# Optimization experiments

Measured on AMD Instinct MI355X. Metric: run time of the kernel, lower is better.

Reference implementation:

```python
import jax, jax.numpy as jnp
import numpy as np

N_NODES = 50000
N_EDGES = 800000
IN_CH = 128
HID_CH = 128
OUT_CH = 64
K = 25
LRELU_SLOPE = 0.01  # torch.nn.LeakyReLU default
NORM_EPS = 1e-12    # F.normalize default eps


def setup_inputs() -> dict:
    key = jax.random.key(0)
    ks = jax.random.split(key, 8)
    x = jax.random.normal(ks[0], (N_NODES, IN_CH), dtype=jnp.float32)
    edge_index = jax.random.randint(ks[1], (2, N_EDGES), 0, N_NODES, dtype=jnp.int32)
    # ChebConv per-order weights [K, in, hid] + bias
    W = jax.random.normal(ks[2], (K, IN_CH, HID_CH), dtype=jnp.float32) / np.sqrt(IN_CH)
    b = jax.random.normal(ks[3], (HID_CH,), dtype=jnp.float32) * 0.01
    # mu / logstd linear heads
    w_mu = jax.random.normal(ks[4], (HID_CH, OUT_CH), dtype=jnp.float32) / np.sqrt(HID_CH)
    b_mu = jax.random.normal(ks[5], (OUT_CH,), dtype=jnp.float32) * 0.01
    w_ls = jax.random.normal(ks[6], (HID_CH, OUT_CH), dtype=jnp.float32) / np.sqrt(HID_CH)
    b_ls = jax.random.normal(ks[7], (OUT_CH,), dtype=jnp.float32) * 0.01
    return {"x": x, "edge_index": edge_index, "W": W, "b": b,
            "w_mu": w_mu, "b_mu": b_mu, "w_ls": w_ls, "b_ls": b_ls}


def _cheb_conv(x, edge_index, W, b):
    # PyG ChebConv with normalization='sym', lambda_max=2.0:
    # scaled Laplacian L~ = L - I = -D^{-1/2} A D^{-1/2} (diagonal nets to zero)
    src, dst = edge_index[0], edge_index[1]
    deg = jax.ops.segment_sum(jnp.ones(src.shape[0], x.dtype), src, num_segments=x.shape[0])
    dis = jnp.where(deg > 0, jax.lax.rsqrt(jnp.where(deg > 0, deg, 1.0)), 0.0)
    enorm = -dis[src] * dis[dst]  # [E]

    def prop(h):  # out[i] = sum_{(j->i)} enorm_e * h[j]
        return jax.ops.segment_sum(enorm[:, None] * h[src], dst, num_segments=h.shape[0])

    tx0 = x
    tx1 = prop(x)
    out0 = tx0 @ W[0] + tx1 @ W[1]

    def step(carry, Wk):
        t1, t0, acc = carry
        t2 = 2.0 * prop(t1) - t0  # Chebyshev recurrence
        return (t2, t1, acc + t2 @ Wk), None

    (_, _, out), _ = jax.lax.scan(step, (tx1, tx0, out0), W[2:])
    return out + b


def reference(x, edge_index, W, b, w_mu, b_mu, w_ls, b_ls):
    h = _cheb_conv(x, edge_index, W, b)
    # eval mode: dropout is identity
    h = jnp.where(h > 0, h, LRELU_SLOPE * h)
    mu = h @ w_mu + b_mu
    ls = h @ w_ls + b_ls
    nrm = jnp.sqrt(jnp.sum(ls * ls, axis=1, keepdims=True))
    logstd = ls / jnp.maximum(nrm, NORM_EPS) * 1.8
    zeta = mu  # eval-mode reparam returns mu
    return (mu, logstd, zeta)
```

## Files before the change

### kernel.cpp

```cpp
#include <hip/hip_runtime.h>
#include <hip/hip_fp16.h>

#define N_NODES 50000
#define N_EDGES 800000
#define CH 128
#define OUT_CH 64
#define K_ORD 25
#define SLICE ((size_t)N_NODES * CH)

typedef __attribute__((ext_vector_type(8))) short s16x8;
typedef __attribute__((ext_vector_type(4))) float f32x4;

union U4H8 { uint4 u; __half2 h2[4]; ushort us[8]; };

__global__ void count_kernel(const int* __restrict__ ei, float* __restrict__ deg,
                             int* __restrict__ indeg, int E) {
    int e = blockIdx.x * blockDim.x + threadIdx.x;
    if (e >= E) return;
    int s = ei[e];
    int d = ei[E + e];
    atomicAdd(&deg[s], 1.0f);
    atomicAdd(&indeg[d], 1);
}

__global__ __launch_bounds__(256) void scan1_kernel(const int* __restrict__ indeg,
                                                    int* __restrict__ loc,
                                                    int* __restrict__ bsum, int n) {
    __shared__ int tmp[256];
    int tid = threadIdx.x;
    int i = blockIdx.x * 256 + tid;
    int v = (i < n) ? indeg[i] : 0;
    tmp[tid] = v;
    __syncthreads();
    for (int off = 1; off < 256; off <<= 1) {
        int t = (tid >= off) ? tmp[tid - off] : 0;
        __syncthreads();
        tmp[tid] += t;
        __syncthreads();
    }
    if (i < n) loc[i] = tmp[tid] - v;
    if (tid == 255) bsum[blockIdx.x] = tmp[255];
}

__global__ __launch_bounds__(256) void scan2_kernel(int* __restrict__ bsum, int nb) {
    __shared__ int tmp[256];
    int tid = threadIdx.x;
    int v = (tid < nb) ? bsum[tid] : 0;
    tmp[tid] = v;
    __syncthreads();
    for (int off = 1; off < 256; off <<= 1) {
        int t = (tid >= off) ? tmp[tid - off] : 0;
        __syncthreads();
        tmp[tid] += t;
        __syncthreads();
    }
    if (tid < nb) bsum[tid] = tmp[tid] - v;
    if (tid == 255) bsum[nb] = tmp[255];
}

__global__ __launch_bounds__(256) void scan3_kernel(const int* __restrict__ loc,
                                                    const int* __restrict__ bsum,
                                                    int* __restrict__ rowptr,
                                                    int* __restrict__ cursor, int n, int nb) {
    int i = blockIdx.x * 256 + threadIdx.x;
    if (i < n) {
        int r = loc[i] + bsum[i >> 8];
        rowptr[i] = r;
        cursor[i] = r;
    }
    if (i == n) rowptr[n] = bsum[nb];
}

__global__ void scatter_kernel(const int* __restrict__ ei, const float* __restrict__ deg,
                               int* __restrict__ cursor, int* __restrict__ col,
                               float* __restrict__ ew, int E) {
    int e = blockIdx.x * blockDim.x + threadIdx.x;
    if (e >= E) return;
    int s = ei[e];
    int d = ei[E + e];
    float ds = deg[s], dd = deg[d];
    float dis_s = ds > 0.f ? rsqrtf(ds) : 0.f;
    float dis_d = dd > 0.f ? rsqrtf(dd) : 0.f;
    int pos = atomicAdd(&cursor[d], 1);
    col[pos] = s;
    ew[pos] = -dis_s * dis_d;
}

__global__ __launch_bounds__(256) void cvt_kernel(const float* __restrict__ in,
                                                  ushort* __restrict__ out, int n8) {
    int i = blockIdx.x * 256 + threadIdx.x;
    if (i >= n8) return;
    float4 a = ((const float4*)in)[2 * i];
    float4 b = ((const float4*)in)[2 * i + 1];
    U4H8 p;
    p.h2[0] = __float22half2_rn(make_float2(a.x, a.y));
    p.h2[1] = __float22half2_rn(make_float2(a.z, a.w));
    p.h2[2] = __float22half2_rn(make_float2(b.x, b.y));
    p.h2[3] = __float22half2_rn(make_float2(b.z, b.w));
    ((uint4*)out)[i] = p.u;
}

__global__ __launch_bounds__(256) void wprep_kernel(const float* __restrict__ W,
                                                    ushort* __restrict__ WT) {
    int idx = blockIdx.x * 256 + threadIdx.x;
    if (idx >= K_ORD * 128 * 32) return;
    int c4 = idx & 31;
    int nrow = (idx >> 5) & 127;
    int k = idx >> 12;
    const float* Wk = W + (size_t)k * CH * CH;
    ushort o[4];
    #pragma unroll
    for (int j = 0; j < 4; ++j)
        o[j] = __half_as_ushort(__float2half_rn(Wk[(c4 * 4 + j) * CH + nrow]));
    *(ushort2*)(WT + (size_t)k * CH * CH + nrow * CH + c4 * 4)     = make_ushort2(o[0], o[1]);
    *(ushort2*)(WT + (size_t)k * CH * CH + nrow * CH + c4 * 4 + 2) = make_ushort2(o[2], o[3]);
}

__global__ __launch_bounds__(256) void prop_kernel(
    const ushort* __restrict__ tin, const ushort* __restrict__ tprev,
    ushort* __restrict__ tout, const int* __restrict__ rowptr,
    const int* __restrict__ col, const float* __restrict__ ew, int n, int mode) {
    int wid = blockIdx.x * 4 + (threadIdx.x >> 6);
    if (wid >= n) return;
    int lane = threadIdx.x & 63;
    int g = lane >> 4, sub = lane & 15;
    int beg = rowptr[wid], end = rowptr[wid + 1];
    float acc[8] = {0.f, 0.f, 0.f, 0.f, 0.f, 0.f, 0.f, 0.f};
    for (int e0 = beg; e0 < end; e0 += 64) {
        int ne = min(64, end - e0);
        int c = 0; float w = 0.f;
        if (lane < ne) { c = col[e0 + lane]; w = ew[e0 + lane]; }
        for (int j16 = 0; j16 < ne; j16 += 16) {
            U4H8 v[4];
            float wj[4];
            #pragma unroll
            for (int u = 0; u < 4; ++u) {
                int j = j16 + u * 4 + g;
                int cj = __shfl(c, j & 63);
                float wf = __shfl(w, j & 63);
                wj[u] = (j < ne) ? wf : 0.f;
                v[u].u = ((const uint4*)(tin + (size_t)cj * CH))[sub];
            }
            #pragma unroll
            for (int u = 0; u < 4; ++u) {
                #pragma unroll
                for (int t = 0; t < 4; ++t) {
                    float2 f = __half22float2(v[u].h2[t]);
                    acc[2 * t]     = fmaf(wj[u], f.x, acc[2 * t]);
                    acc[2 * t + 1] = fmaf(wj[u], f.y, acc[2 * t + 1]);
                }
            }
        }
    }
    #pragma unroll
    for (int i = 0; i < 8; ++i) {
        acc[i] += __shfl_xor(acc[i], 16);
        acc[i] += __shfl_xor(acc[i], 32);
    }
    if (g == 0) {
        size_t base = (size_t)wid * CH + sub * 8;
        float r[8];
        if (mode) {
            U4H8 pv;
            pv.u = *(const uint4*)(tprev + base);
            #pragma unroll
            for (int t = 0; t < 4; ++t) {
                float2 f = __half22float2(pv.h2[t]);
                r[2 * t]     = 2.f * acc[2 * t]     - f.x;
                r[2 * t + 1] = 2.f * acc[2 * t + 1] - f.y;
            }
        } else {
            #pragma unroll
            for (int i = 0; i < 8; ++i) r[i] = acc[i];
        }
        U4H8 p;
        p.h2[0] = __float22half2_rn(make_float2(r[0], r[1]));
        p.h2[1] = __float22half2_rn(make_float2(r[2], r[3]));
        p.h2[2] = __float22half2_rn(make_float2(r[4], r[5]));
        p.h2[3] = __float22half2_rn(make_float2(r[6], r[7]));
        *(uint4*)(tout + base) = p.u;
    }
}

__global__ __launch_bounds__(256) void gemm_kernel(
    const ushort* __restrict__ T, size_t slice_stride, const ushort* __restrict__ WT,
    float* __restrict__ C, int M, int k0, int nk, int beta) {
    __shared__ ushort As[128 * 128];
    __shared__ ushort Ws[128 * 128];
    int tid = threadIdx.x;
    int row0 = blockIdx.x * 128;
    int wave = tid >> 6, lane = tid & 63;
    int wrow = wave * 32;
    int lr = lane & 15, kg = lane >> 4;

    f32x4 acc[2][8];
    #pragma unroll
    for (int a = 0; a < 2; ++a)
        #pragma unroll
        for (int c = 0; c < 8; ++c)
            acc[a][c] = (f32x4){0.f, 0.f, 0.f, 0.f};

    for (int ks = 0; ks < nk; ++ks) {
        const ushort* Ak = T + (size_t)(k0 + ks) * slice_stride;
        const ushort* Wk = WT + (size_t)(k0 + ks) * (CH * CH);
        #pragma unroll
        for (int i = 0; i < 8; ++i) {
            int idx = tid + i * 256;
            int r = idx >> 4, gg = idx & 15;
            uint4 v = make_uint4(0u, 0u, 0u, 0u);
            int gr = row0 + r;
            if (gr < M) v = ((const uint4*)(Ak + (size_t)gr * CH))[gg];
            int gs = gg ^ (r & 15);
            *(uint4*)(&As[r * 128 + gs * 8]) = v;
        }
        #pragma unroll
        for (int i = 0; i < 8; ++i) {
            int idx = tid + i * 256;
            int r = idx >> 4, gg = idx & 15;
            uint4 v = ((const uint4*)(Wk + (size_t)r * CH))[gg];
            int gs = gg ^ (r & 15);
            *(uint4*)(&Ws[r * 128 + gs * 8]) = v;
        }
        __syncthreads();

        #pragma unroll
        for (int kc = 0; kc < 4; ++kc) {
            int gbase = kc * 4 + kg;
            int gs = gbase ^ lr;
            s16x8 a0 = *(const s16x8*)(&As[(wrow + lr) * 128 + gs * 8]);
            s16x8 a1 = *(const s16x8*)(&As[(wrow + 16 + lr) * 128 + gs * 8]);
            #pragma unroll
            for (int c = 0; c < 8; ++c) {
                s16x8 bfr = *(const s16x8*)(&Ws[(c * 16 + lr) * 128 + gs * 8]);
                acc[0][c] = __builtin_amdgcn_mfma_f32_16x16x32_f16(a0, bfr, acc[0][c], 0, 0, 0);
                acc[1][c] = __builtin_amdgcn_mfma_f32_16x16x32_f16(a1, bfr, acc[1][c], 0, 0, 0);
            }
        }
        __syncthreads();
    }

    #pragma unroll
    for (int rf = 0; rf < 2; ++rf)
        #pragma unroll
        for (int c = 0; c < 8; ++c)
            #pragma unroll
            for (int j = 0; j < 4; ++j) {
                int gr = row0 + wrow + rf * 16 + kg * 4 + j;
                int gc = c * 16 + lr;
                if (gr < M) {
                    float v = acc[rf][c][j];
                    if (beta) v += C[(size_t)gr * 128 + gc];
                    C[(size_t)gr * 128 + gc] = v;
                }
            }
}

__global__ __launch_bounds__(256) void head_kernel(
    const float* __restrict__ acc_in, const float* __restrict__ b,
    const float* __restrict__ w_mu, const float* __restrict__ b_mu,
    const float* __restrict__ w_ls, const float* __restrict__ b_ls,
    float* __restrict__ out, int M) {
    __shared__ ushort Hs[128 * 128];
    __shared__ ushort Ws[128 * 128];
    __shared__ float s_b[128];
    int tid = threadIdx.x;
    int row0 = blockIdx.x * 128;
    if (tid < 128) s_b[tid] = b[tid];
    __syncthreads();

    #pragma unroll
    for (int i = 0; i < 16; ++i) {
        int idx = tid + i * 256;
        int r = idx >> 5, c4 = idx & 31;
        float4 v = make_float4(0.f, 0.f, 0.f, 0.f);
        int gr = row0 + r;
        if (gr < M) v = ((const float4*)(acc_in + (size_t)gr * CH))[c4];
        float hv[4] = { v.x, v.y, v.z, v.w };
        #pragma unroll
        for (int j = 0; j < 4; ++j) {
            float h = hv[j] + s_b[c4 * 4 + j];
            hv[j] = h > 0.f ? h : 0.01f * h;
        }
        __half2 p0 = __float22half2_rn(make_float2(hv[0], hv[1]));
        __half2 p1 = __float22half2_rn(make_float2(hv[2], hv[3]));
        int gg = c4 >> 1, hh = c4 & 1;
        int gs = gg ^ (r & 15);
        uint2 pk;
        pk.x = *(unsigned int*)&p0;
        pk.y = *(unsigned int*)&p1;
        *(uint2*)(&Hs[r * 128 + gs * 8 + hh * 4]) = pk;
    }
    #pragma unroll
    for (int i = 0; i < 16; ++i) {
        int idx = tid + i * 256;
        int k = idx >> 5, n4 = idx & 31;
        const float* src = (n4 < 16) ? w_mu : w_ls;
        float4 v = ((const float4*)src)[k * 16 + (n4 & 15)];
        int gk = k >> 3, kk = k & 7;
        float vv[4] = { v.x, v.y, v.z, v.w };
        #pragma unroll
        for (int j = 0; j < 4; ++j) {
            int nn = n4 * 4 + j;
            int gs = gk ^ (nn & 15);
            Ws[nn * 128 + gs * 8 + kk] = __half_as_ushort(__float2half_rn(vv[j]));
        }
    }
    __syncthreads();

    int wave = tid >> 6, lane = tid & 63;
    int wrow = wave * 32;
    int lr = lane & 15, kg = lane >> 4;
    f32x4 acc[2][8];
    #pragma unroll
    for (int a = 0; a < 2; ++a)
        #pragma unroll
        for (int c = 0; c < 8; ++c)
            acc[a][c] = (f32x4){0.f, 0.f, 0.f, 0.f};

    #pragma unroll
    for (int kc = 0; kc < 4; ++kc) {
        int gbase = kc * 4 + kg;
        int gs = gbase ^ lr;
        s16x8 a0 = *(const s16x8*)(&Hs[(wrow + lr) * 128 + gs * 8]);
        s16x8 a1 = *(const s16x8*)(&Hs[(wrow + 16 + lr) * 128 + gs * 8]);
        #pragma unroll
        for (int c = 0; c < 8; ++c) {
            s16x8 bfr = *(const s16x8*)(&Ws[(c * 16 + lr) * 128 + gs * 8]);
            acc[0][c] = __builtin_amdgcn_mfma_f32_16x16x32_f16(a0, bfr, acc[0][c], 0, 0, 0);
            acc[1][c] = __builtin_amdgcn_mfma_f32_16x16x32_f16(a1, bfr, acc[1][c], 0, 0, 0);
        }
    }

    #pragma unroll
    for (int rf = 0; rf < 2; ++rf)
        #pragma unroll
        for (int j = 0; j < 4; ++j) {
            int gr = row0 + wrow + rf * 16 + kg * 4 + j;
            float muv[4], lsv[4];
            float s2 = 0.f;
            #pragma unroll
            for (int c = 0; c < 4; ++c) {
                muv[c] = acc[rf][c][j] + b_mu[c * 16 + lr];
                float l = acc[rf][4 + c][j] + b_ls[c * 16 + lr];
                lsv[c] = l;
                s2 = fmaf(l, l, s2);
            }
            s2 += __shfl_xor(s2, 1);
            s2 += __shfl_xor(s2, 2);
            s2 += __shfl_xor(s2, 4);
            s2 += __shfl_xor(s2, 8);
            float sc = 1.8f / fmaxf(sqrtf(s2), 1e-12f);
            if (gr < M) {
                size_t base = (size_t)gr * OUT_CH;
                #pragma unroll
                for (int c = 0; c < 4; ++c) {
                    int gc = c * 16 + lr;
                    out[base + gc] = muv[c];
                    out[(size_t)N_NODES * OUT_CH + base + gc] = lsv[c] * sc;
                    out[2 * (size_t)N_NODES * OUT_CH + base + gc] = muv[c];
                }
            }
        }
}

extern "C" void kernel_launch(void* const* d_in, const int* in_sizes, int n_in,
                              void* d_out, int out_size, void* d_ws, size_t ws_size,
                              hipStream_t stream) {
    const float* x    = (const float*)d_in[0];
    const int*   ei   = (const int*)d_in[1];
    const float* W    = (const float*)d_in[2];
    const float* b    = (const float*)d_in[3];
    const float* w_mu = (const float*)d_in[4];
    const float* b_mu = (const float*)d_in[5];
    const float* w_ls = (const float*)d_in[6];
    const float* b_ls = (const float*)d_in[7];

    const int N = N_NODES, E = N_EDGES;
    const int NB = (N + 255) / 256;
    char* p = (char*)d_ws;
    auto alloc = [&](size_t bytes) {
        char* r = p;
        p += (bytes + 511) & ~(size_t)511;
        return r;
    };
    float*  deg    = (float*)alloc((size_t)N * 4);
    int*    indeg  = (int*)alloc((size_t)N * 4);
    int*    rowptr = (int*)alloc((size_t)(N + 1) * 4);
    int*    cursor = (int*)alloc((size_t)N * 4);
    int*    loc    = (int*)alloc((size_t)N * 4);
    int*    bsum   = (int*)alloc((size_t)(NB + 1) * 4);
    int*    col    = (int*)alloc((size_t)E * 4);
    float*  ew     = (float*)alloc((size_t)E * 4);
    ushort* WT     = (ushort*)alloc((size_t)K_ORD * CH * CH * 2);
    float*  accbuf = (float*)alloc((size_t)N * CH * 4);

    size_t used = (size_t)(p - (char*)d_ws);
    bool bigpath = ws_size >= used + (size_t)K_ORD * SLICE * 2 + (1u << 20);

    hipMemsetAsync(deg, 0, (size_t)N * 4, stream);
    hipMemsetAsync(indeg, 0, (size_t)N * 4, stream);

    count_kernel<<<(E + 255) / 256, 256, 0, stream>>>(ei, deg, indeg, E);
    scan1_kernel<<<NB, 256, 0, stream>>>(indeg, loc, bsum, N);
    scan2_kernel<<<1, 256, 0, stream>>>(bsum, NB);
    scan3_kernel<<<NB, 256, 0, stream>>>(loc, bsum, rowptr, cursor, N, NB);
    scatter_kernel<<<(E + 255) / 256, 256, 0, stream>>>(ei, deg, cursor, col, ew, E);
    wprep_kernel<<<(K_ORD * 128 * 32 + 255) / 256, 256, 0, stream>>>(W, WT);

    int gemm_grid = (N + 127) / 128;
    int prop_grid = (N + 3) / 4;
    int cvt_grid = (N * 16 + 255) / 256;

    if (bigpath) {
        ushort* T = (ushort*)alloc((size_t)K_ORD * SLICE * 2);
        cvt_kernel<<<cvt_grid, 256, 0, stream>>>(x, T, N * 16);
        prop_kernel<<<prop_grid, 256, 0, stream>>>(T, T, T + SLICE,
                                                   rowptr, col, ew, N, 0);
        for (int k = 2; k < K_ORD; ++k)
            prop_kernel<<<prop_grid, 256, 0, stream>>>(
                T + (size_t)(k - 1) * SLICE, T + (size_t)(k - 2) * SLICE,
                T + (size_t)k * SLICE, rowptr, col, ew, N, 1);
        gemm_kernel<<<gemm_grid, 256, 0, stream>>>(T, SLICE, WT, accbuf, N, 0, K_ORD, 0);
    } else {
        ushort* r0 = (ushort*)alloc(SLICE * 2);
        ushort* r1 = (ushort*)alloc(SLICE * 2);
        ushort* r2 = (ushort*)alloc(SLICE * 2);
        ushort* Ss[3] = { r0, r1, r2 };
        cvt_kernel<<<cvt_grid, 256, 0, stream>>>(x, r0, N * 16);
        gemm_kernel<<<gemm_grid, 256, 0, stream>>>(r0, 0, WT, accbuf, N, 0, 1, 0);
        prop_kernel<<<prop_grid, 256, 0, stream>>>(r0, r0, r1, rowptr, col, ew, N, 0);
        gemm_kernel<<<gemm_grid, 256, 0, stream>>>(r1, 0, WT, accbuf, N, 1, 1, 1);
        for (int k = 2; k < K_ORD; ++k) {
            prop_kernel<<<prop_grid, 256, 0, stream>>>(
                Ss[(k - 1) % 3], Ss[(k - 2) % 3], Ss[k % 3], rowptr, col, ew, N, 1);
            gemm_kernel<<<gemm_grid, 256, 0, stream>>>(Ss[k % 3], 0, WT, accbuf, N, k, 1, 1);
        }
    }

    head_kernel<<<gemm_grid, 256, 0, stream>>>(accbuf, b, w_mu, b_mu, w_ls, b_ls,
                                               (float*)d_out, N);
}
```

Baseline: 1.503 ms.

## Fuse Chebyshev propagation steps into one cooperative kernel with grid syncs

Replaces the fp16 conversion and the 24 separate prop_kernel launches with one cooperative persistent kernel of 1024 blocks. Each block owns 49 nodes and runs all recurrence orders, separated by grid.sync. Each block keeps its own nodes' previous-order values in shared memory, so the t_{k-2} term is not re-read from global memory. This removes per-launch overhead and tail effects, but adds grid-wide barrier cost, a fixed node partition that can be load-imbalanced, and lower occupancy than the original launches.

```diff
diff --git a/kernel.cpp b/kernel.cpp
--- a/kernel.cpp
+++ b/kernel.cpp
@@ -1,5 +1,8 @@
 #include <hip/hip_runtime.h>
 #include <hip/hip_fp16.h>
+#include <hip/hip_cooperative_groups.h>
+
+namespace cg = cooperative_groups;
 
 #define N_NODES 50000
 #define N_EDGES 800000
@@ -7,6 +10,8 @@
 #define OUT_CH 64
 #define K_ORD 25
 #define SLICE ((size_t)N_NODES * CH)
+#define NPB 49
+#define GRID_C 1024
 
 typedef __attribute__((ext_vector_type(8))) short s16x8;
 typedef __attribute__((ext_vector_type(4))) float f32x4;
@@ -114,6 +119,96 @@
         o[j] = __half_as_ushort(__float2half_rn(Wk[(c4 * 4 + j) * CH + nrow]));
     *(ushort2*)(WT + (size_t)k * CH * CH + nrow * CH + c4 * 4)     = make_ushort2(o[0], o[1]);
     *(ushort2*)(WT + (size_t)k * CH * CH + nrow * CH + c4 * 4 + 2) = make_ushort2(o[2], o[3]);
+}
+
+__global__ __launch_bounds__(256) void cheb_kernel(
+    const float* __restrict__ x, ushort* __restrict__ T,
+    const int* __restrict__ rowptr, const int* __restrict__ col,
+    const float* __restrict__ ew, int n) {
+    cg::grid_group grid = cg::this_grid();
+    __shared__ ushort pv[2][NPB][CH];
+    int tid = threadIdx.x;
+    int wv = tid >> 6, lane = tid & 63;
+    int gq = lane >> 4, sub = lane & 15;
+    int nbase = blockIdx.x * NPB;
+
+    for (int ln = wv; ln < NPB; ln += 4) {
+        int nid = nbase + ln;
+        if (nid >= n) break;
+        float2 f = ((const float2*)(x + (size_t)nid * CH))[lane];
+        __half2 h = __float22half2_rn(f);
+        unsigned int u = *(unsigned int*)&h;
+        *(unsigned int*)&pv[0][ln][lane * 2] = u;
+        *(unsigned int*)(T + (size_t)nid * CH + lane * 2) = u;
+    }
+    grid.sync();
+
+    for (int k = 1; k < K_ORD; ++k) {
+        const ushort* tin = T + (size_t)(k - 1) * SLICE;
+        ushort* tout = T + (size_t)k * SLICE;
+        int pb = k & 1;
+        for (int ln = wv; ln < NPB; ln += 4) {
+            int nid = nbase + ln;
+            if (nid >= n) break;
+            int beg = rowptr[nid], end = rowptr[nid + 1];
+            float acc[8] = {0.f, 0.f, 0.f, 0.f, 0.f, 0.f, 0.f, 0.f};
+            for (int e0 = beg; e0 < end; e0 += 64) {
+                int ne = min(64, end - e0);
+                int c = 0; float w = 0.f;
+                if (lane < ne) { c = col[e0 + lane]; w = ew[e0 + lane]; }
+                for (int j16 = 0; j16 < ne; j16 += 16) {
+                    U4H8 v[4];
+                    float wj[4];
+                    #pragma unroll
+                    for (int u = 0; u < 4; ++u) {
+                        int j = j16 + u * 4 + gq;
+                        int cj = __shfl(c, j & 63);
+                        float wf = __shfl(w, j & 63);
+                        wj[u] = (j < ne) ? wf : 0.f;
+                        v[u].u = ((const uint4*)(tin + (size_t)cj * CH))[sub];
+                    }
+                    #pragma unroll
+                    for (int u = 0; u < 4; ++u) {
+                        #pragma unroll
+                        for (int t = 0; t < 4; ++t) {
+                            float2 f = __half22float2(v[u].h2[t]);
+                            acc[2 * t]     = fmaf(wj[u], f.x, acc[2 * t]);
+                            acc[2 * t + 1] = fmaf(wj[u], f.y, acc[2 * t + 1]);
+                        }
+                    }
+                }
+            }
+            #pragma unroll
+            for (int i = 0; i < 8; ++i) {
+                acc[i] += __shfl_xor(acc[i], 16);
+                acc[i] += __shfl_xor(acc[i], 32);
+            }
+            if (gq == 0) {
+                float r[8];
+                if (k == 1) {
+                    #pragma unroll
+                    for (int i = 0; i < 8; ++i) r[i] = acc[i];
+                } else {
+                    U4H8 pvv;
+                    pvv.u = *(const uint4*)&pv[pb][ln][sub * 8];
+                    #pragma unroll
+                    for (int t = 0; t < 4; ++t) {
+                        float2 f = __half22float2(pvv.h2[t]);
+                        r[2 * t]     = 2.f * acc[2 * t]     - f.x;
+                        r[2 * t + 1] = 2.f * acc[2 * t + 1] - f.y;
+                    }
+                }
+                U4H8 p;
+                p.h2[0] = __float22half2_rn(make_float2(r[0], r[1]));
+                p.h2[1] = __float22half2_rn(make_float2(r[2], r[3]));
+                p.h2[2] = __float22half2_rn(make_float2(r[4], r[5]));
+                p.h2[3] = __float22half2_rn(make_float2(r[6], r[7]));
+                *(uint4*)&pv[pb][ln][sub * 8] = p.u;
+                *(uint4*)(tout + (size_t)nid * CH + sub * 8) = p.u;
+            }
+        }
+        grid.sync();
+    }
 }
 
 __global__ __launch_bounds__(256) void prop_kernel(
@@ -413,13 +508,11 @@
 
     if (bigpath) {
         ushort* T = (ushort*)alloc((size_t)K_ORD * SLICE * 2);
-        cvt_kernel<<<cvt_grid, 256, 0, stream>>>(x, T, N * 16);
-        prop_kernel<<<prop_grid, 256, 0, stream>>>(T, T, T + SLICE,
-                                                   rowptr, col, ew, N, 0);
-        for (int k = 2; k < K_ORD; ++k)
-            prop_kernel<<<prop_grid, 256, 0, stream>>>(
-                T + (size_t)(k - 1) * SLICE, T + (size_t)(k - 2) * SLICE,
-                T + (size_t)k * SLICE, rowptr, col, ew, N, 1);
+        int nn = N;
+        void* args[] = { (void*)&x, (void*)&T, (void*)&rowptr,
+                         (void*)&col, (void*)&ew, (void*)&nn };
+        (void)hipLaunchCooperativeKernel((void*)cheb_kernel, dim3(GRID_C), dim3(256),
+                                         args, 0, stream);
         gemm_kernel<<<gemm_grid, 256, 0, stream>>>(T, SLICE, WT, accbuf, N, 0, K_ORD, 0);
     } else {
         ushort* r0 = (ushort*)alloc(SLICE * 2);
```

Measured after the change: 1.503 ms. About the same (-0.1%).

## Rescale Chebyshev basis by degree to drop per-edge weights in propagation

Applied to the files above, without the earlier changes.

Reformulates the symmetric-normalized propagation in a degree-rescaled basis (T scaled by D^{-1/2}), so each edge contributes an unweighted sum. The per-edge weight array and its shuffle and load disappear, and one per-node scale is applied at the end of each row. The GEMM rescales rows back by sqrt(deg) when staging A tiles. This saves edge-weight bandwidth in the hot gather loop. In exchange it adds a per-element convert and multiply in the GEMM load path and changes fp16 rounding behaviour, since values scaled by degree may have a different dynamic range.

```diff
diff --git a/kernel.cpp b/kernel.cpp
--- a/kernel.cpp
+++ b/kernel.cpp
@@ -13,13 +13,13 @@
 
 union U4H8 { uint4 u; __half2 h2[4]; ushort us[8]; };
 
-__global__ void count_kernel(const int* __restrict__ ei, float* __restrict__ deg,
+__global__ void count_kernel(const int* __restrict__ ei, int* __restrict__ deg_i,
                              int* __restrict__ indeg, int E) {
     int e = blockIdx.x * blockDim.x + threadIdx.x;
     if (e >= E) return;
     int s = ei[e];
     int d = ei[E + e];
-    atomicAdd(&deg[s], 1.0f);
+    atomicAdd(&deg_i[s], 1);
     atomicAdd(&indeg[d], 1);
 }
 
@@ -71,32 +71,49 @@
     if (i == n) rowptr[n] = bsum[nb];
 }
 
-__global__ void scatter_kernel(const int* __restrict__ ei, const float* __restrict__ deg,
-                               int* __restrict__ cursor, int* __restrict__ col,
-                               float* __restrict__ ew, int E) {
+__global__ void scatter_kernel(const int* __restrict__ ei, int* __restrict__ cursor,
+                               int* __restrict__ col, int E) {
     int e = blockIdx.x * blockDim.x + threadIdx.x;
     if (e >= E) return;
     int s = ei[e];
     int d = ei[E + e];
-    float ds = deg[s], dd = deg[d];
-    float dis_s = ds > 0.f ? rsqrtf(ds) : 0.f;
-    float dis_d = dd > 0.f ? rsqrtf(dd) : 0.f;
     int pos = atomicAdd(&cursor[d], 1);
     col[pos] = s;
-    ew[pos] = -dis_s * dis_d;
+}
+
+__global__ __launch_bounds__(256) void scaleprep_kernel(const int* __restrict__ deg_i,
+                                                        float* __restrict__ beta,
+                                                        float* __restrict__ alpha,
+                                                        float* __restrict__ gam, int n) {
+    int i = blockIdx.x * 256 + threadIdx.x;
+    if (i >= n) return;
+    int dg = deg_i[i];
+    if (dg > 0) {
+        float fd = (float)dg;
+        beta[i] = -2.f / fd;
+        alpha[i] = rsqrtf(fd);
+        gam[i] = sqrtf(fd);
+    } else {
+        beta[i] = 0.f;
+        alpha[i] = 1.f;
+        gam[i] = 1.f;
+    }
 }
 
 __global__ __launch_bounds__(256) void cvt_kernel(const float* __restrict__ in,
+                                                  const float* __restrict__ alpha,
                                                   ushort* __restrict__ out, int n8) {
     int i = blockIdx.x * 256 + threadIdx.x;
     if (i >= n8) return;
+    int row = i >> 4;
+    float al = alpha[row];
     float4 a = ((const float4*)in)[2 * i];
     float4 b = ((const float4*)in)[2 * i + 1];
     U4H8 p;
-    p.h2[0] = __float22half2_rn(make_float2(a.x, a.y));
-    p.h2[1] = __float22half2_rn(make_float2(a.z, a.w));
-    p.h2[2] = __float22half2_rn(make_float2(b.x, b.y));
-    p.h2[3] = __float22half2_rn(make_float2(b.z, b.w));
+    p.h2[0] = __float22half2_rn(make_float2(al * a.x, al * a.y));
+    p.h2[1] = __float22half2_rn(make_float2(al * a.z, al * a.w));
+    p.h2[2] = __float22half2_rn(make_float2(al * b.x, al * b.y));
+    p.h2[3] = __float22half2_rn(make_float2(al * b.z, al * b.w));
     ((uint4*)out)[i] = p.u;
 }
 
@@ -119,7 +136,7 @@
 __global__ __launch_bounds__(256) void prop_kernel(
     const ushort* __restrict__ tin, const ushort* __restrict__ tprev,
     ushort* __restrict__ tout, const int* __restrict__ rowptr,
-    const int* __restrict__ col, const float* __restrict__ ew, int n, int mode) {
+    const int* __restrict__ col, const float* __restrict__ beta, int n, int mode) {
     int wid = blockIdx.x * 4 + (threadIdx.x >> 6);
     if (wid >= n) return;
     int lane = threadIdx.x & 63;
@@ -128,17 +145,16 @@
     float acc[8] = {0.f, 0.f, 0.f, 0.f, 0.f, 0.f, 0.f, 0.f};
     for (int e0 = beg; e0 < end; e0 += 64) {
         int ne = min(64, end - e0);
-        int c = 0; float w = 0.f;
-        if (lane < ne) { c = col[e0 + lane]; w = ew[e0 + lane]; }
+        int c = 0;
+        if (lane < ne) c = col[e0 + lane];
         for (int j16 = 0; j16 < ne; j16 += 16) {
             U4H8 v[4];
-            float wj[4];
+            float m[4];
             #pragma unroll
             for (int u = 0; u < 4; ++u) {
                 int j = j16 + u * 4 + g;
                 int cj = __shfl(c, j & 63);
-                float wf = __shfl(w, j & 63);
-                wj[u] = (j < ne) ? wf : 0.f;
+                m[u] = (j < ne) ? 1.f : 0.f;
                 v[u].u = ((const uint4*)(tin + (size_t)cj * CH))[sub];
             }
             #pragma unroll
@@ -146,8 +162,8 @@
                 #pragma unroll
                 for (int t = 0; t < 4; ++t) {
                     float2 f = __half22float2(v[u].h2[t]);
-                    acc[2 * t]     = fmaf(wj[u], f.x, acc[2 * t]);
-                    acc[2 * t + 1] = fmaf(wj[u], f.y, acc[2 * t + 1]);
+                    acc[2 * t]     = fmaf(m[u], f.x, acc[2 * t]);
+                    acc[2 * t + 1] = fmaf(m[u], f.y, acc[2 * t + 1]);
                 }
             }
         }
@@ -158,6 +174,7 @@
         acc[i] += __shfl_xor(acc[i], 32);
     }
     if (g == 0) {
+        float bt = beta[wid];
         size_t base = (size_t)wid * CH + sub * 8;
         float r[8];
         if (mode) {
@@ -166,12 +183,13 @@
             #pragma unroll
             for (int t = 0; t < 4; ++t) {
                 float2 f = __half22float2(pv.h2[t]);
-                r[2 * t]     = 2.f * acc[2 * t]     - f.x;
-                r[2 * t + 1] = 2.f * acc[2 * t + 1] - f.y;
+                r[2 * t]     = fmaf(bt, acc[2 * t],     -f.x);
+                r[2 * t + 1] = fmaf(bt, acc[2 * t + 1], -f.y);
             }
         } else {
-            #pragma unroll
-            for (int i = 0; i < 8; ++i) r[i] = acc[i];
+            float hb = 0.5f * bt;
+            #pragma unroll
+            for (int i = 0; i < 8; ++i) r[i] = hb * acc[i];
         }
         U4H8 p;
         p.h2[0] = __float22half2_rn(make_float2(r[0], r[1]));
@@ -183,8 +201,9 @@
 }
 
 __global__ __launch_bounds__(256) void gemm_kernel(
-    const ushort* __restrict__ T, size_t slice_stride, const ushort* __restrict__ WT,
-    float* __restrict__ C, int M, int k0, int nk, int beta) {
+    const ushort* __restrict__ T, size_t kstride, const ushort* __restrict__ WT,
+    const float* __restrict__ gam, float* __restrict__ C,
+    int M, int wk0, int nk, int betaf) {
     __shared__ ushort As[128 * 128];
     __shared__ ushort Ws[128 * 128];
     int tid = threadIdx.x;
@@ -201,17 +220,26 @@
             acc[a][c] = (f32x4){0.f, 0.f, 0.f, 0.f};
 
     for (int ks = 0; ks < nk; ++ks) {
-        const ushort* Ak = T + (size_t)(k0 + ks) * slice_stride;
-        const ushort* Wk = WT + (size_t)(k0 + ks) * (CH * CH);
+        const ushort* Ak = T + (size_t)ks * kstride;
+        const ushort* Wk = WT + (size_t)(wk0 + ks) * (CH * CH);
         #pragma unroll
         for (int i = 0; i < 8; ++i) {
             int idx = tid + i * 256;
             int r = idx >> 4, gg = idx & 15;
-            uint4 v = make_uint4(0u, 0u, 0u, 0u);
             int gr = row0 + r;
-            if (gr < M) v = ((const uint4*)(Ak + (size_t)gr * CH))[gg];
+            U4H8 hv;
+            hv.u = make_uint4(0u, 0u, 0u, 0u);
+            if (gr < M) {
+                hv.u = ((const uint4*)(Ak + (size_t)gr * CH))[gg];
+                float gm = gam[gr];
+                #pragma unroll
+                for (int t = 0; t < 4; ++t) {
+                    float2 f = __half22float2(hv.h2[t]);
+                    hv.h2[t] = __float22half2_rn(make_float2(gm * f.x, gm * f.y));
+                }
+            }
             int gs = gg ^ (r & 15);
-            *(uint4*)(&As[r * 128 + gs * 8]) = v;
+            *(uint4*)(&As[r * 128 + gs * 8]) = hv.u;
         }
         #pragma unroll
         for (int i = 0; i < 8; ++i) {
@@ -249,7 +277,7 @@
                 int gc = c * 16 + lr;
                 if (gr < M) {
                     float v = acc[rf][c][j];
-                    if (beta) v += C[(size_t)gr * 128 + gc];
+                    if (betaf) v += C[(size_t)gr * 128 + gc];
                     C[(size_t)gr * 128 + gc] = v;
                 }
             }
@@ -383,28 +411,31 @@
         p += (bytes + 511) & ~(size_t)511;
         return r;
     };
-    float*  deg    = (float*)alloc((size_t)N * 4);
+    int*    deg_i  = (int*)alloc((size_t)N * 4);
     int*    indeg  = (int*)alloc((size_t)N * 4);
     int*    rowptr = (int*)alloc((size_t)(N + 1) * 4);
     int*    cursor = (int*)alloc((size_t)N * 4);
     int*    loc    = (int*)alloc((size_t)N * 4);
     int*    bsum   = (int*)alloc((size_t)(NB + 1) * 4);
     int*    col    = (int*)alloc((size_t)E * 4);
-    float*  ew     = (float*)alloc((size_t)E * 4);
+    float*  beta   = (float*)alloc((size_t)N * 4);
+    float*  alpha  = (float*)alloc((size_t)N * 4);
+    float*  gam    = (float*)alloc((size_t)N * 4);
     ushort* WT     = (ushort*)alloc((size_t)K_ORD * CH * CH * 2);
     float*  accbuf = (float*)alloc((size_t)N * CH * 4);
 
     size_t used = (size_t)(p - (char*)d_ws);
     bool bigpath = ws_size >= used + (size_t)K_ORD * SLICE * 2 + (1u << 20);
 
-    hipMemsetAsync(deg, 0, (size_t)N * 4, stream);
-    hipMemsetAsync(indeg, 0, (size_t)N * 4, stream);
-
-    count_kernel<<<(E + 255) / 256, 256, 0, stream>>>(ei, deg, indeg, E);
+    (void)hipMemsetAsync(deg_i, 0, (size_t)N * 4, stream);
+    (void)hipMemsetAsync(indeg, 0, (size_t)N * 4, stream);
+
+    count_kernel<<<(E + 255) / 256, 256, 0, stream>>>(ei, deg_i, indeg, E);
     scan1_kernel<<<NB, 256, 0, stream>>>(indeg, loc, bsum, N);
     scan2_kernel<<<1, 256, 0, stream>>>(bsum, NB);
     scan3_kernel<<<NB, 256, 0, stream>>>(loc, bsum, rowptr, cursor, N, NB);
-    scatter_kernel<<<(E + 255) / 256, 256, 0, stream>>>(ei, deg, cursor, col, ew, E);
+    scatter_kernel<<<(E + 255) / 256, 256, 0, stream>>>(ei, cursor, col, E);
+    scaleprep_kernel<<<(N + 255) / 256, 256, 0, stream>>>(deg_i, beta, alpha, gam, N);
     wprep_kernel<<<(K_ORD * 128 * 32 + 255) / 256, 256, 0, stream>>>(W, WT);
 
     int gemm_grid = (N + 127) / 128;
@@ -413,27 +444,29 @@
 
     if (bigpath) {
         ushort* T = (ushort*)alloc((size_t)K_ORD * SLICE * 2);
-        cvt_kernel<<<cvt_grid, 256, 0, stream>>>(x, T, N * 16);
+        cvt_kernel<<<cvt_grid, 256, 0, stream>>>(x, alpha, T, N * 16);
         prop_kernel<<<prop_grid, 256, 0, stream>>>(T, T, T + SLICE,
-                                                   rowptr, col, ew, N, 0);
+                                                   rowptr, col, beta, N, 0);
         for (int k = 2; k < K_ORD; ++k)
             prop_kernel<<<prop_grid, 256, 0, stream>>>(
                 T + (size_t)(k - 1) * SLICE, T + (size_t)(k - 2) * SLICE,
-                T + (size_t)k * SLICE, rowptr, col, ew, N, 1);
-        gemm_kernel<<<gemm_grid, 256, 0, stream>>>(T, SLICE, WT, accbuf, N, 0, K_ORD, 0);
+                T + (size_t)k * SLICE, rowptr, col, beta, N, 1);
+        gemm_kernel<<<gemm_grid, 256, 0, stream>>>(T, SLICE, WT, gam, accbuf,
+                                                   N, 0, K_ORD, 0);
     } else {
         ushort* r0 = (ushort*)alloc(SLICE * 2);
         ushort* r1 = (ushort*)alloc(SLICE * 2);
         ushort* r2 = (ushort*)alloc(SLICE * 2);
         ushort* Ss[3] = { r0, r1, r2 };
-        cvt_kernel<<<cvt_grid, 256, 0, stream>>>(x, r0, N * 16);
-        gemm_kernel<<<gemm_grid, 256, 0, stream>>>(r0, 0, WT, accbuf, N, 0, 1, 0);
-        prop_kernel<<<prop_grid, 256, 0, stream>>>(r0, r0, r1, rowptr, col, ew, N, 0);
-        gemm_kernel<<<gemm_grid, 256, 0, stream>>>(r1, 0, WT, accbuf, N, 1, 1, 1);
+        cvt_kernel<<<cvt_grid, 256, 0, stream>>>(x, alpha, r0, N * 16);
+        gemm_kernel<<<gemm_grid, 256, 0, stream>>>(r0, 0, WT, gam, accbuf, N, 0, 1, 0);
+        prop_kernel<<<prop_grid, 256, 0, stream>>>(r0, r0, r1, rowptr, col, beta, N, 0);
+        gemm_kernel<<<gemm_grid, 256, 0, stream>>>(r1, 0, WT, gam, accbuf, N, 1, 1, 1);
         for (int k = 2; k < K_ORD; ++k) {
             prop_kernel<<<prop_grid, 256, 0, stream>>>(
-                Ss[(k - 1) % 3], Ss[(k - 2) % 3], Ss[k % 3], rowptr, col, ew, N, 1);
-            gemm_kernel<<<gemm_grid, 256, 0, stream>>>(Ss[k % 3], 0, WT, accbuf, N, k, 1, 1);
+                Ss[(k - 1) % 3], Ss[(k - 2) % 3], Ss[k % 3], rowptr, col, beta, N, 1);
+            gemm_kernel<<<gemm_grid, 256, 0, stream>>>(Ss[k % 3], 0, WT, gam, accbuf,
+                                                       N, k, 1, 1);
         }
     }
 
```

Result: no change. 1.516 ms (+0.8%).
